# Kernel tuning notes

Measured on AMD Instinct MI355X. Metric: run time of the kernel, lower is better.

## Reference

```python
import jax, jax.numpy as jnp
import numpy as np

B, S, K, N, G = 2, 2048, 4096, 11008, 128  # tokens=B*S, group_size=G

def setup_inputs() -> dict:
    key = jax.random.key(0)
    k1, k2, k3, k4 = jax.random.split(key, 4)
    x = jax.random.normal(k1, (B, S, K), dtype=jnp.float16)
    # packed INT4 weights: one uint8 holds two nibbles along N (even col = low nibble)
    w_packed = jax.random.randint(k2, (K, N // 2), 0, 256, dtype=jnp.int32).astype(jnp.uint8)
    # realistic per-group scales (small positive) and integer zeros in [0,16)
    w_scale = (jax.random.uniform(k3, (K // G, N), dtype=jnp.float32) * 0.02 + 1e-3).astype(jnp.float16)
    w_zero = jax.random.randint(k4, (K // G, N), 0, 16).astype(jnp.float16)
    return {"x": x, "w_packed": w_packed, "w_scale": w_scale, "w_zero": w_zero}

def reference(x, w_packed, w_scale, w_zero):
    Kd, Nh = w_packed.shape  # [K, N//2]
    # unpack nibbles: even output column = low nibble, odd = high nibble
    low = (w_packed & 0xF).astype(jnp.float16)
    high = ((w_packed >> 4) & 0xF).astype(jnp.float16)
    w_int4 = jnp.stack([low, high], axis=-1).reshape(Kd, 2 * Nh)  # [K, N]
    # per-group dequant: group index = k // G along the K axis
    scale = jnp.repeat(w_scale, G, axis=0)  # [K, N]
    zero = jnp.repeat(w_zero, G, axis=0)    # [K, N]
    w = (w_int4 - zero) * scale             # fp16 dequantized weight [K, N]
    x2 = x.reshape(-1, Kd)                  # [M, K]
    # fp16 inputs, fp32 accumulation (matches tl.dot acc fp32), store fp16
    acc = jnp.einsum('mk,kn->mn', x2, w, preferred_element_type=jnp.float32)
    out = acc.astype(jnp.float16)
    return out.reshape(*x.shape[:-1], 2 * Nh)
```

## Files before the change

kernel.cpp:

```cpp
#include <hip/hip_runtime.h>
#include <hip/hip_bf16.h>
#include <stdint.h>

typedef __bf16 bf16_t;
typedef __bf16 bf16x8 __attribute__((ext_vector_type(8)));
typedef float floatx4 __attribute__((ext_vector_type(4)));
typedef uint32_t u32;

#define M_DIM 4096
#define K_DIM 4096
#define N_DIM 11008
#define GRP 128
#define NHALF (N_DIM / 2)
#define NTILES (N_DIM / 16)
#define KB32 (K_DIM / 32)
#define WB_DWORDS (NTILES * KB32 * 64)
#define WB_BYTES ((size_t)WB_DWORDS * 4)

__global__ __launch_bounds__(256) void repack_w_kernel(const int* __restrict__ wp,
                                                       u32* __restrict__ WB) {
  const u32 o     = blockIdx.x * 256u + threadIdx.x;
  const u32 lane  = o & 63u;
  const u32 kblk  = (o >> 6) & (KB32 - 1);
  const u32 ntile = o >> 13;
  const u32 n     = ntile * 16u + (lane & 15u);
  const u32 nh    = n >> 1;
  const u32 sh    = (n & 1u) * 4u;
  const u32 kbase = kblk * 32u + (lane >> 4) * 8u;
  const int* src  = wp + (size_t)kbase * NHALF + nh;
  u32 d = 0;
#pragma unroll
  for (int j = 0; j < 8; ++j) {
    u32 v = (u32)src[(size_t)j * NHALF];
    d |= ((v >> sh) & 0xFu) << (4 * j);
  }
  WB[o] = d;
}

__global__ __launch_bounds__(256) void gemm_int4_kernel(const float* __restrict__ x,
                                                        const u32* __restrict__ WB,
                                                        const float* __restrict__ wscale,
                                                        const float* __restrict__ wzero,
                                                        float* __restrict__ out) {
  __shared__ __align__(16) bf16_t As[128 * 64];

  const u32 tid  = threadIdx.x;
  const u32 lane = tid & 63u;
  const u32 wave = tid >> 6;
  const u32 l15  = lane & 15u;
  const u32 quad = lane >> 4;

  const u32 n0 = blockIdx.x * 128u;
  const u32 m0 = blockIdx.y * 128u;

  const float* xsrc = x + (m0 + (tid >> 3)) * (u32)K_DIM + (tid & 7u) * 8u;
  char* lds_dst = (char*)(&As[0]) + tid * 16u;

  const u32* wb_base = WB + ((n0 >> 4) + wave * 2u) * (u32)(KB32 * 64) + lane;
  const u32 n_idx    = n0 + wave * 32u + l15;

  const bf16_t* afrag_base = &As[0] + l15 * 64u + quad * 8u;

  floatx4 acc[8][2];
  floatx4 zero4 = {0.f, 0.f, 0.f, 0.f};
#pragma unroll
  for (int i = 0; i < 8; ++i)
#pragma unroll
    for (int t = 0; t < 2; ++t) acc[i][t] = zero4;

  float sc[2], zs[2];

  for (u32 kt = 0; kt < K_DIM / 64u; ++kt) {
    const float* src = xsrc + kt * 64u;
    bf16x8 av[4];
#pragma unroll
    for (int it = 0; it < 4; ++it) {
      float4 f0 = *(const float4*)(src + it * 32 * K_DIM);
      float4 f1 = *(const float4*)(src + it * 32 * K_DIM + 4);
      bf16x8 v;
      v[0] = (bf16_t)f0.x; v[1] = (bf16_t)f0.y; v[2] = (bf16_t)f0.z; v[3] = (bf16_t)f0.w;
      v[4] = (bf16_t)f1.x; v[5] = (bf16_t)f1.y; v[6] = (bf16_t)f1.z; v[7] = (bf16_t)f1.w;
      av[it] = v;
    }

    u32 bq[2][2];
#pragma unroll
    for (int ks = 0; ks < 2; ++ks)
#pragma unroll
      for (int t = 0; t < 2; ++t)
        bq[ks][t] = wb_base[(u32)(t * KB32 * 64) + (kt * 2u + ks) * 64u];

    if ((kt & 1u) == 0u) {
      const u32 g = kt >> 1;
#pragma unroll
      for (int t = 0; t < 2; ++t) {
        float s = wscale[g * N_DIM + n_idx + t * 16u];
        float z = wzero[g * N_DIM + n_idx + t * 16u];
        sc[t] = s;
        zs[t] = s * z;
      }
    }

    __syncthreads();
#pragma unroll
    for (int it = 0; it < 4; ++it)
      *(bf16x8*)(lds_dst + it * 4096) = av[it];
    __syncthreads();

#pragma unroll
    for (int ks = 0; ks < 2; ++ks) {
      bf16x8 af[8];
#pragma unroll
      for (int i = 0; i < 8; ++i)
        af[i] = *(const bf16x8*)(afrag_base + i * 16 * 64 + ks * 32);
#pragma unroll
      for (int t = 0; t < 2; ++t) {
        bf16x8 bfr;
#pragma unroll
        for (int j = 0; j < 8; ++j) {
          float w = (float)((bq[ks][t] >> (4 * j)) & 0xFu) * sc[t] - zs[t];
          bfr[j] = (bf16_t)w;
        }
#pragma unroll
        for (int i = 0; i < 8; ++i)
          acc[i][t] = __builtin_amdgcn_mfma_f32_16x16x32_bf16(af[i], bfr, acc[i][t], 0, 0, 0);
      }
    }
  }

  const u32 col0 = n0 + wave * 32u + l15;
  const u32 row0 = m0 + quad * 4u;
#pragma unroll
  for (int i = 0; i < 8; ++i)
#pragma unroll
    for (int t = 0; t < 2; ++t)
#pragma unroll
      for (int r = 0; r < 4; ++r)
        out[(row0 + i * 16u + r) * (u32)N_DIM + col0 + t * 16u] = acc[i][t][r];
}

__global__ __launch_bounds__(256) void gemm_int4_direct(const float* __restrict__ x,
                                                        const int* __restrict__ wp,
                                                        const float* __restrict__ wscale,
                                                        const float* __restrict__ wzero,
                                                        float* __restrict__ out) {
  __shared__ __align__(16) bf16_t As[128 * 64];
  __shared__ unsigned char Wb[64 * 68];

  const u32 tid  = threadIdx.x;
  const u32 lane = tid & 63u;
  const u32 wave = tid >> 6;
  const u32 l15  = lane & 15u;
  const u32 quad = lane >> 4;

  const u32 n0 = blockIdx.x * 128u;
  const u32 m0 = blockIdx.y * 128u;

  const float* xsrc = x + (m0 + (tid >> 3)) * (u32)K_DIM + (tid & 7u) * 8u;
  char* lds_dst = (char*)(&As[0]) + tid * 16u;

  const u32 wrow = tid >> 2;
  const u32 wcol = (tid & 3u) * 16;
  const int* wsrc = wp + (size_t)wrow * NHALF + (n0 >> 1) + wcol;

  const u32 n_idx = n0 + wave * 32u + l15;
  const u32 bcol0 = (wave * 32u + l15) >> 1;
  const u32 bcol1 = (wave * 32u + 16u + l15) >> 1;
  const u32 nsh   = (l15 & 1u) * 4u;

  floatx4 acc[8][2];
  floatx4 zero4 = {0.f, 0.f, 0.f, 0.f};
#pragma unroll
  for (int i = 0; i < 8; ++i)
#pragma unroll
    for (int t = 0; t < 2; ++t) acc[i][t] = zero4;

  const bf16_t* afrag_base = &As[0] + l15 * 64u + quad * 8u;
  float sc[2], zs[2];

  for (u32 kt = 0; kt < K_DIM / 64u; ++kt) {
    const float* src = xsrc + kt * 64u;
    bf16x8 av[4];
#pragma unroll
    for (int it = 0; it < 4; ++it) {
      float4 f0 = *(const float4*)(src + it * 32 * K_DIM);
      float4 f1 = *(const float4*)(src + it * 32 * K_DIM + 4);
      bf16x8 v;
      v[0] = (bf16_t)f0.x; v[1] = (bf16_t)f0.y; v[2] = (bf16_t)f0.z; v[3] = (bf16_t)f0.w;
      v[4] = (bf16_t)f1.x; v[5] = (bf16_t)f1.y; v[6] = (bf16_t)f1.z; v[7] = (bf16_t)f1.w;
      av[it] = v;
    }

    const int* wsk = wsrc + (size_t)kt * 64u * NHALF;
    int4 wv[4];
#pragma unroll
    for (int q = 0; q < 4; ++q) wv[q] = *(const int4*)(wsk + q * 4);

    if ((kt & 1u) == 0u) {
      const u32 g = kt >> 1;
#pragma unroll
      for (int t = 0; t < 2; ++t) {
        float s = wscale[g * N_DIM + n_idx + t * 16u];
        float z = wzero[g * N_DIM + n_idx + t * 16u];
        sc[t] = s;
        zs[t] = s * z;
      }
    }

    __syncthreads();
#pragma unroll
    for (int it = 0; it < 4; ++it)
      *(bf16x8*)(lds_dst + it * 4096) = av[it];
#pragma unroll
    for (int q = 0; q < 4; ++q) {
      u32 d = ((u32)wv[q].x & 0xFFu) | (((u32)wv[q].y & 0xFFu) << 8) |
              (((u32)wv[q].z & 0xFFu) << 16) | (((u32)wv[q].w & 0xFFu) << 24);
      *(u32*)(&Wb[wrow * 68u + wcol + q * 4u]) = d;
    }
    __syncthreads();

#pragma unroll
    for (int ks = 0; ks < 2; ++ks) {
      bf16x8 af[8];
#pragma unroll
      for (int i = 0; i < 8; ++i)
        af[i] = *(const bf16x8*)(afrag_base + i * 16 * 64 + ks * 32);
#pragma unroll
      for (int t = 0; t < 2; ++t) {
        const u32 bc = t ? bcol1 : bcol0;
        bf16x8 bfr;
#pragma unroll
        for (int j = 0; j < 8; ++j) {
          u32 byte = Wb[(ks * 32u + quad * 8u + j) * 68u + bc];
          float w = (float)((byte >> nsh) & 0xFu) * sc[t] - zs[t];
          bfr[j] = (bf16_t)w;
        }
#pragma unroll
        for (int i = 0; i < 8; ++i)
          acc[i][t] = __builtin_amdgcn_mfma_f32_16x16x32_bf16(af[i], bfr, acc[i][t], 0, 0, 0);
      }
    }
  }

  const u32 col0 = n0 + wave * 32u + l15;
  const u32 row0 = m0 + quad * 4u;
#pragma unroll
  for (int i = 0; i < 8; ++i)
#pragma unroll
    for (int t = 0; t < 2; ++t)
#pragma unroll
      for (int r = 0; r < 4; ++r)
        out[(row0 + i * 16u + r) * (u32)N_DIM + col0 + t * 16u] = acc[i][t][r];
}

extern "C" void kernel_launch(void* const* d_in, const int* in_sizes, int n_in,
                              void* d_out, int out_size, void* d_ws, size_t ws_size,
                              hipStream_t stream) {
  const float* x      = (const float*)d_in[0];
  const int*   wp     = (const int*)d_in[1];
  const float* wscale = (const float*)d_in[2];
  const float* wzero  = (const float*)d_in[3];
  float*       out    = (float*)d_out;

  if (ws_size >= WB_BYTES && d_ws != nullptr) {
    u32* WB = (u32*)d_ws;
    repack_w_kernel<<<WB_DWORDS / 256, 256, 0, stream>>>(wp, WB);
    gemm_int4_kernel<<<dim3(N_DIM / 128, M_DIM / 128), 256, 0, stream>>>(x, WB, wscale, wzero, out);
  } else {
    gemm_int4_direct<<<dim3(N_DIM / 128, M_DIM / 128), 256, 0, stream>>>(x, wp, wscale, wzero, out);
  }
}
```

Baseline: 805.1 us.

## Switch GEMM to fp16 MFMA with magic-number dequant, 2x2 wave tiling and swizzled LDS

Moves the main GEMM from bf16 to fp16 MFMA. Weights are dequantized with the 0x6400 magic-number trick and packed half2 arithmetic in place of per-element float conversions. Waves are rearranged into a 2x2 grid of 64x64 tiles, which changes the A/B fragment reuse, and the A tile in LDS uses an XOR swizzle to avoid bank conflicts. The repack kernel is rewritten to stage weights through shared memory with coalesced loads and an interleaved nibble order, so each lane can read 16 bytes of weights at once. Scale and zero are rounded to fp16, which costs some precision in the dequant.

```diff
diff --git a/kernel.cpp b/kernel.cpp
--- a/kernel.cpp
+++ b/kernel.cpp
@@ -4,6 +4,9 @@
 
 typedef __bf16 bf16_t;
 typedef __bf16 bf16x8 __attribute__((ext_vector_type(8)));
+typedef _Float16 f16;
+typedef _Float16 f16x8 __attribute__((ext_vector_type(8)));
+typedef _Float16 h2 __attribute__((ext_vector_type(2)));
 typedef float floatx4 __attribute__((ext_vector_type(4)));
 typedef uint32_t u32;
 
@@ -12,29 +15,55 @@
 #define N_DIM 11008
 #define GRP 128
 #define NHALF (N_DIM / 2)
-#define NTILES (N_DIM / 16)
-#define KB32 (K_DIM / 32)
-#define WB_DWORDS (NTILES * KB32 * 64)
+#define N64T (N_DIM / 64)
+#define KTN (K_DIM / 64)
+#define WB_DWORDS (N64T * KTN * 64 * 8)
 #define WB_BYTES ((size_t)WB_DWORDS * 4)
 
 __global__ __launch_bounds__(256) void repack_w_kernel(const int* __restrict__ wp,
                                                        u32* __restrict__ WB) {
-  const u32 o     = blockIdx.x * 256u + threadIdx.x;
-  const u32 lane  = o & 63u;
-  const u32 kblk  = (o >> 6) & (KB32 - 1);
-  const u32 ntile = o >> 13;
-  const u32 n     = ntile * 16u + (lane & 15u);
-  const u32 nh    = n >> 1;
-  const u32 sh    = (n & 1u) * 4u;
-  const u32 kbase = kblk * 32u + (lane >> 4) * 8u;
-  const int* src  = wp + (size_t)kbase * NHALF + nh;
-  u32 d = 0;
-#pragma unroll
-  for (int j = 0; j < 8; ++j) {
-    u32 v = (u32)src[(size_t)j * NHALF];
-    d |= ((v >> sh) & 0xFu) << (4 * j);
-  }
-  WB[o] = d;
+  __shared__ unsigned char Wt[64][36];
+
+  const u32 tid = threadIdx.x;
+  const u32 n64 = blockIdx.x;
+  const u32 kt  = blockIdx.y;
+
+  {
+    const u32 r = tid >> 2;
+    const u32 c = (tid & 3u) * 8u;
+    const int* src = wp + (size_t)(kt * 64u + r) * NHALF + n64 * 32u + c;
+    int4 a = *(const int4*)(src);
+    int4 b = *(const int4*)(src + 4);
+    u32 lo = ((u32)a.x & 0xFFu) | (((u32)a.y & 0xFFu) << 8) |
+             (((u32)a.z & 0xFFu) << 16) | (((u32)a.w & 0xFFu) << 24);
+    u32 hi = ((u32)b.x & 0xFFu) | (((u32)b.y & 0xFFu) << 8) |
+             (((u32)b.z & 0xFFu) << 16) | (((u32)b.w & 0xFFu) << 24);
+    *(u32*)&Wt[r][c]      = lo;
+    *(u32*)&Wt[r][c + 4u] = hi;
+  }
+  __syncthreads();
+
+  const u32 tt    = tid & 3u;
+  const u32 ks    = (tid >> 2) & 1u;
+  const u32 lane0 = tid >> 3;
+  const u32 l15   = lane0 & 15u;
+  const u32 cb    = tt * 8u + (l15 >> 1);
+  const u32 sh    = (l15 & 1u) * 4u;
+  const size_t obase = ((size_t)(n64 * 64u + kt) * 64u) * 8u;
+
+#pragma unroll
+  for (int half = 0; half < 2; ++half) {
+    const u32 lane = lane0 + (u32)half * 32u;
+    const u32 kb   = ks * 32u + (lane >> 4) * 8u;
+    u32 d = 0;
+#pragma unroll
+    for (int p = 0; p < 8; ++p) {
+      const int j = (p < 4) ? (2 * p) : (2 * (p - 4) + 1);
+      u32 byte = Wt[kb + (u32)j][cb];
+      d |= ((byte >> sh) & 0xFu) << (4 * p);
+    }
+    WB[obase + tid + (u32)half * 256u] = d;
+  }
 }
 
 __global__ __launch_bounds__(256) void gemm_int4_kernel(const float* __restrict__ x,
@@ -42,101 +71,119 @@
                                                         const float* __restrict__ wscale,
                                                         const float* __restrict__ wzero,
                                                         float* __restrict__ out) {
-  __shared__ __align__(16) bf16_t As[128 * 64];
+  __shared__ __align__(16) f16 As[128 * 64];
 
   const u32 tid  = threadIdx.x;
   const u32 lane = tid & 63u;
   const u32 wave = tid >> 6;
   const u32 l15  = lane & 15u;
   const u32 quad = lane >> 4;
+  const u32 wr   = wave >> 1;
+  const u32 wc   = wave & 1u;
 
   const u32 n0 = blockIdx.x * 128u;
   const u32 m0 = blockIdx.y * 128u;
 
-  const float* xsrc = x + (m0 + (tid >> 3)) * (u32)K_DIM + (tid & 7u) * 8u;
-  char* lds_dst = (char*)(&As[0]) + tid * 16u;
-
-  const u32* wb_base = WB + ((n0 >> 4) + wave * 2u) * (u32)(KB32 * 64) + lane;
-  const u32 n_idx    = n0 + wave * 32u + l15;
-
-  const bf16_t* afrag_base = &As[0] + l15 * 64u + quad * 8u;
-
-  floatx4 acc[8][2];
+  const u32 srow  = tid >> 3;
+  const u32 sslot = tid & 7u;
+  const float* xsrc = x + (size_t)(m0 + srow) * K_DIM + sslot * 8u;
+  char* lds_dst = (char*)As + srow * 128u + ((sslot ^ (srow & 7u)) * 16u);
+
+  const u32* wb_base = WB + ((size_t)((n0 >> 6) + wc) * KTN * 64u) * 8u + lane * 8u;
+
+  const u32 arow = wr * 64u + l15;
+  const f16* a0 = As + arow * 64u + (((quad)      ^ (l15 & 7u)) * 8u);
+  const f16* a1 = As + arow * 64u + (((4u + quad) ^ (l15 & 7u)) * 8u);
+
+  floatx4 acc[4][4];
   floatx4 zero4 = {0.f, 0.f, 0.f, 0.f};
 #pragma unroll
-  for (int i = 0; i < 8; ++i)
-#pragma unroll
-    for (int t = 0; t < 2; ++t) acc[i][t] = zero4;
-
-  float sc[2], zs[2];
-
-  for (u32 kt = 0; kt < K_DIM / 64u; ++kt) {
+  for (int i = 0; i < 4; ++i)
+#pragma unroll
+    for (int t = 0; t < 4; ++t) acc[i][t] = zero4;
+
+  h2 s2[4], z2[4];
+  const u32 nidx0 = n0 + wc * 64u + l15;
+
+  for (u32 kt = 0; kt < KTN; ++kt) {
     const float* src = xsrc + kt * 64u;
-    bf16x8 av[4];
+    f16x8 av[4];
 #pragma unroll
     for (int it = 0; it < 4; ++it) {
-      float4 f0 = *(const float4*)(src + it * 32 * K_DIM);
-      float4 f1 = *(const float4*)(src + it * 32 * K_DIM + 4);
-      bf16x8 v;
-      v[0] = (bf16_t)f0.x; v[1] = (bf16_t)f0.y; v[2] = (bf16_t)f0.z; v[3] = (bf16_t)f0.w;
-      v[4] = (bf16_t)f1.x; v[5] = (bf16_t)f1.y; v[6] = (bf16_t)f1.z; v[7] = (bf16_t)f1.w;
-      av[it] = v;
-    }
-
-    u32 bq[2][2];
-#pragma unroll
-    for (int ks = 0; ks < 2; ++ks)
-#pragma unroll
-      for (int t = 0; t < 2; ++t)
-        bq[ks][t] = wb_base[(u32)(t * KB32 * 64) + (kt * 2u + ks) * 64u];
+      float4 f0 = *(const float4*)(src + (size_t)it * 32 * K_DIM);
+      float4 f1 = *(const float4*)(src + (size_t)it * 32 * K_DIM + 4);
+      union { f16x8 v; h2 h[4]; } u;
+      u.h[0] = __builtin_bit_cast(h2, __builtin_amdgcn_cvt_pkrtz(f0.x, f0.y));
+      u.h[1] = __builtin_bit_cast(h2, __builtin_amdgcn_cvt_pkrtz(f0.z, f0.w));
+      u.h[2] = __builtin_bit_cast(h2, __builtin_amdgcn_cvt_pkrtz(f1.x, f1.y));
+      u.h[3] = __builtin_bit_cast(h2, __builtin_amdgcn_cvt_pkrtz(f1.z, f1.w));
+      av[it] = u.v;
+    }
+
+    const u32* wp8 = wb_base + (size_t)kt * 512u;
+    uint4 bq0 = *(const uint4*)(wp8);
+    uint4 bq1 = *(const uint4*)(wp8 + 4u);
 
     if ((kt & 1u) == 0u) {
       const u32 g = kt >> 1;
 #pragma unroll
-      for (int t = 0; t < 2; ++t) {
-        float s = wscale[g * N_DIM + n_idx + t * 16u];
-        float z = wzero[g * N_DIM + n_idx + t * 16u];
-        sc[t] = s;
-        zs[t] = s * z;
+      for (int t = 0; t < 4; ++t) {
+        float s = wscale[g * N_DIM + nidx0 + (u32)t * 16u];
+        float z = wzero [g * N_DIM + nidx0 + (u32)t * 16u];
+        f16 sh_ = (f16)s;
+        f16 zh_ = (f16)(1024.0f + z);
+        h2 sv = {sh_, sh_};
+        h2 zv = {zh_, zh_};
+        s2[t] = sv;
+        z2[t] = zv;
       }
     }
 
     __syncthreads();
 #pragma unroll
     for (int it = 0; it < 4; ++it)
-      *(bf16x8*)(lds_dst + it * 4096) = av[it];
+      *(f16x8*)(lds_dst + it * 4096) = av[it];
     __syncthreads();
 
 #pragma unroll
     for (int ks = 0; ks < 2; ++ks) {
-      bf16x8 af[8];
-#pragma unroll
-      for (int i = 0; i < 8; ++i)
-        af[i] = *(const bf16x8*)(afrag_base + i * 16 * 64 + ks * 32);
-#pragma unroll
-      for (int t = 0; t < 2; ++t) {
-        bf16x8 bfr;
-#pragma unroll
-        for (int j = 0; j < 8; ++j) {
-          float w = (float)((bq[ks][t] >> (4 * j)) & 0xFu) * sc[t] - zs[t];
-          bfr[j] = (bf16_t)w;
-        }
-#pragma unroll
-        for (int i = 0; i < 8; ++i)
-          acc[i][t] = __builtin_amdgcn_mfma_f32_16x16x32_bf16(af[i], bfr, acc[i][t], 0, 0, 0);
+      f16x8 af[4];
+      const f16* ab = ks ? a1 : a0;
+#pragma unroll
+      for (int i = 0; i < 4; ++i)
+        af[i] = *(const f16x8*)(ab + i * 16 * 64);
+
+      const uint4 bqv = ks ? bq1 : bq0;
+      const u32 qs[4] = {bqv.x, bqv.y, bqv.z, bqv.w};
+#pragma unroll
+      for (int t = 0; t < 4; ++t) {
+        const u32 q = qs[t];
+        u32 w01 = (q & 0x000F000Fu) | 0x64006400u;
+        u32 w23 = ((q >> 4) & 0x000F000Fu) | 0x64006400u;
+        u32 w45 = ((q >> 8) & 0x000F000Fu) | 0x64006400u;
+        u32 w67 = ((q >> 12) & 0x000F000Fu) | 0x64006400u;
+        union { f16x8 v; h2 h[4]; } bf;
+        bf.h[0] = (__builtin_bit_cast(h2, w01) - z2[t]) * s2[t];
+        bf.h[1] = (__builtin_bit_cast(h2, w23) - z2[t]) * s2[t];
+        bf.h[2] = (__builtin_bit_cast(h2, w45) - z2[t]) * s2[t];
+        bf.h[3] = (__builtin_bit_cast(h2, w67) - z2[t]) * s2[t];
+#pragma unroll
+        for (int i = 0; i < 4; ++i)
+          acc[i][t] = __builtin_amdgcn_mfma_f32_16x16x32_f16(af[i], bf.v, acc[i][t], 0, 0, 0);
       }
     }
   }
 
-  const u32 col0 = n0 + wave * 32u + l15;
-  const u32 row0 = m0 + quad * 4u;
-#pragma unroll
-  for (int i = 0; i < 8; ++i)
-#pragma unroll
-    for (int t = 0; t < 2; ++t)
+  const u32 col0 = n0 + wc * 64u + l15;
+  const u32 row0 = m0 + wr * 64u + quad * 4u;
+#pragma unroll
+  for (int i = 0; i < 4; ++i)
+#pragma unroll
+    for (int t = 0; t < 4; ++t)
 #pragma unroll
       for (int r = 0; r < 4; ++r)
-        out[(row0 + i * 16u + r) * (u32)N_DIM + col0 + t * 16u] = acc[i][t][r];
+        out[(size_t)(row0 + (u32)i * 16u + (u32)r) * N_DIM + col0 + (u32)t * 16u] =
+            acc[i][t][r];
 }
 
 __global__ __launch_bounds__(256) void gemm_int4_direct(const float* __restrict__ x,
@@ -264,7 +311,7 @@
 
   if (ws_size >= WB_BYTES && d_ws != nullptr) {
     u32* WB = (u32*)d_ws;
-    repack_w_kernel<<<WB_DWORDS / 256, 256, 0, stream>>>(wp, WB);
+    repack_w_kernel<<<dim3(N64T, KTN), 256, 0, stream>>>(wp, WB);
     gemm_int4_kernel<<<dim3(N_DIM / 128, M_DIM / 128), 256, 0, stream>>>(x, WB, wscale, wzero, out);
   } else {
     gemm_int4_direct<<<dim3(N_DIM / 128, M_DIM / 128), 256, 0, stream>>>(x, wp, wscale, wzero, out);
```

Result: faster. 702.0 us (-12.8%).
